# Kernel tuning notes

Measured on AMD Instinct MI355X. Metric: run time of the kernel, lower is better.

Reference implementation:

```python
import jax, jax.numpy as jnp
import numpy as np

B, P, D = 8, 4096, 3  # B point clouds, P points each, 3-D coords (code slices [:, :3])


def setup_inputs() -> dict:
    key = jax.random.key(0)
    k1, k2 = jax.random.split(key)
    y1 = jax.random.normal(k1, (B * P, D), dtype=jnp.float32)
    y2 = jax.random.normal(k2, (B * P, D), dtype=jnp.float32)
    # Sorted, equal-sized contiguous batch ids (as produced by PyG DataLoader batching).
    b1 = jnp.repeat(jnp.arange(B, dtype=jnp.int32), P)
    b2 = jnp.repeat(jnp.arange(B, dtype=jnp.int32), P)
    return {"y1": y1, "y2": y2, "b1": b1, "b2": b2}


def _chamfer(y1, y2):
    # Batch ids are contiguous with equal counts -> reshape to [B, P, D];
    # knn with batch args restricts neighbors to the same cloud.
    a = y1.reshape(B, P, D)
    c = y2.reshape(B, P, D)
    aa = jnp.sum(a * a, axis=-1)                      # [B, P]
    cc = jnp.sum(c * c, axis=-1)                      # [B, P]
    # Squared pairwise distances per cloud: [B, P, P]
    sq = aa[:, :, None] + cc[:, None, :] - 2.0 * jnp.einsum('bpd,bqd->bpq', a, c)
    # k=1 NN of each y1 point in y2 (argmin over y2 axis)
    idx1 = jnp.argmin(sq, axis=2)                     # [B, P]
    nn1 = jnp.take_along_axis(c, idx1[..., None], axis=1)  # [B, P, D]
    d1 = jnp.mean(jnp.linalg.norm(a - nn1, axis=-1))
    # k=1 NN of each y2 point in y1 (argmin over y1 axis)
    idx2 = jnp.argmin(sq, axis=1)                     # [B, P]
    nn2 = jnp.take_along_axis(a, idx2[..., None], axis=1)  # [B, P, D]
    d2 = jnp.mean(jnp.linalg.norm(c - nn2, axis=-1))
    return d1 + d2


def reference(y1, y2, b1, b2):
    # b1/b2 encode the contiguous equal-size batch structure assumed above.
    return _chamfer(y1, y2)
```

## Files before the change

kernel.cpp:

```cpp
#include <hip/hip_runtime.h>
#include <float.h>
#include <math.h>

#define BB 8
#define PP 4096

typedef __attribute__((ext_vector_type(8))) short bf16x8;
typedef __attribute__((ext_vector_type(16))) float f32x16;

__device__ __forceinline__ unsigned int f2bf(float f) {
    unsigned int u = __float_as_uint(f);
    return (u + 0x7FFFu + ((u >> 16) & 1u)) >> 16;
}
__device__ __forceinline__ float bf2f(unsigned int h) {
    return __uint_as_float(h << 16);
}
__device__ __forceinline__ float min3f(float a, float b, float c) {
    return fminf(fminf(a, b), c);
}

__global__ __launch_bounds__(1024) void chamfer_mfma(
    const float* __restrict__ y1, const float* __restrict__ y2,
    float* __restrict__ partial)
{
    __shared__ uint4 fbuf[64 * 64];

    const int bid   = blockIdx.x;
    const int qg    = bid & 15;
    const int cloud = (bid >> 4) & 7;
    const int dir   = bid >> 7;

    const float* src = (dir == 0) ? y1 : y2;
    const float* tgt = (dir == 0) ? y2 : y1;
    const float* __restrict__ tgt_base = tgt + (size_t)cloud * PP * 3;
    const float* __restrict__ src_base = src + ((size_t)cloud * PP + (size_t)qg * 256) * 3;

    const int tid  = threadIdx.x;
    const int lane = tid & 63;
    const int w    = tid >> 6;
    const int ig   = w & 1;
    const int jg   = w >> 1;

    bf16x8 bfrag[4];
    #pragma unroll
    for (int t = 0; t < 4; ++t) {
        const int ql = (ig * 4 + t) * 32 + (lane & 31);
        const float ax = src_base[ql * 3 + 0];
        const float ay = src_base[ql * 3 + 1];
        const float az = src_base[ql * 3 + 2];
        const unsigned int hx = f2bf(-ax), hy = f2bf(-ay), hz = f2bf(-az);
        const unsigned int lx = f2bf(-ax - bf2f(hx));
        const unsigned int ly = f2bf(-ay - bf2f(hy));
        const unsigned int lz = f2bf(-az - bf2f(hz));
        uint4 bb;
        if (lane < 32) {
            bb.x = hx | (hy << 16);
            bb.y = hz | (lx << 16);
            bb.z = ly | (lz << 16);
            bb.w = hx | (hy << 16);
        } else {
            bb.x = hz | (0x3F80u << 16);
            bb.y = 0x3F80u;
            bb.z = 0u;
            bb.w = 0u;
        }
        bfrag[t] = *reinterpret_cast<bf16x8*>(&bb);
    }

    float m[4][4];
    #pragma unroll
    for (int t = 0; t < 4; ++t)
        #pragma unroll
        for (int r = 0; r < 4; ++r)
            m[t][r] = FLT_MAX;

    f32x16 zc;
    #pragma unroll
    for (int r = 0; r < 16; ++r) zc[r] = 0.0f;

    for (int half = 0; half < 2; ++half) {
        #pragma unroll
        for (int rep = 0; rep < 2; ++rep) {
            const int nl = rep * 1024 + tid;
            const int n  = half * 2048 + nl;
            const float cx = tgt_base[n * 3 + 0];
            const float cy = tgt_base[n * 3 + 1];
            const float cz = tgt_base[n * 3 + 2];
            const unsigned int chx = f2bf(cx), chy = f2bf(cy), chz = f2bf(cz);
            const unsigned int clx = f2bf(cx - bf2f(chx));
            const unsigned int cly = f2bf(cy - bf2f(chy));
            const unsigned int clz = f2bf(cz - bf2f(chz));
            const float hh = 0.5f * (cx * cx + cy * cy + cz * cz);
            const unsigned int hhi = f2bf(hh);
            const unsigned int hlo = f2bf(hh - bf2f(hhi));
            const int tile = nl >> 5, r = nl & 31;
            uint4 lof, hif;
            lof.x = chx | (chy << 16);
            lof.y = chz | (chx << 16);
            lof.z = chy | (chz << 16);
            lof.w = clx | (cly << 16);
            hif.x = clz | (hhi << 16);
            hif.y = hlo;
            hif.z = 0u;
            hif.w = 0u;
            fbuf[tile * 64 + r]      = lof;
            fbuf[tile * 64 + 32 + r] = hif;
        }
        __syncthreads();

        for (int jt = jg * 8; jt < jg * 8 + 8; ++jt) {
            const bf16x8 af = *reinterpret_cast<const bf16x8*>(&fbuf[jt * 64 + lane]);
            #pragma unroll
            for (int t = 0; t < 4; ++t) {
                f32x16 acc = __builtin_amdgcn_mfma_f32_32x32x16_bf16(af, bfrag[t], zc, 0, 0, 0);
                m[t][0] = min3f(m[t][0], acc[0], acc[4]);
                m[t][1] = min3f(m[t][1], acc[1], acc[5]);
                m[t][2] = min3f(m[t][2], acc[2], acc[6]);
                m[t][3] = min3f(m[t][3], acc[3], acc[7]);
                m[t][0] = min3f(m[t][0], acc[8], acc[12]);
                m[t][1] = min3f(m[t][1], acc[9], acc[13]);
                m[t][2] = min3f(m[t][2], acc[10], acc[14]);
                m[t][3] = min3f(m[t][3], acc[11], acc[15]);
            }
        }
        __syncthreads();
    }

    float* pmin = reinterpret_cast<float*>(fbuf);
    float* ssum = pmin + 2048;
    #pragma unroll
    for (int t = 0; t < 4; ++t) {
        float mm = fminf(fminf(m[t][0], m[t][1]), fminf(m[t][2], m[t][3]));
        mm = fminf(mm, __shfl_xor(mm, 32));
        if (lane < 32)
            pmin[jg * 256 + (ig * 4 + t) * 32 + (lane & 31)] = mm;
    }
    __syncthreads();
    if (tid < 256) {
        float v = pmin[tid];
        #pragma unroll
        for (int g = 1; g < 8; ++g)
            v = fminf(v, pmin[g * 256 + tid]);
        const float ax = src_base[tid * 3 + 0];
        const float ay = src_base[tid * 3 + 1];
        const float az = src_base[tid * 3 + 2];
        const float aa = ax * ax + ay * ay + az * az;
        float d = sqrtf(fmaxf(0.0f, fmaf(2.0f, v, aa)));
        #pragma unroll
        for (int off = 32; off > 0; off >>= 1)
            d += __shfl_down(d, off);
        if ((tid & 63) == 0)
            ssum[tid >> 6] = d;
    }
    __syncthreads();
    if (tid == 0)
        partial[bid] = ssum[0] + ssum[1] + ssum[2] + ssum[3];
}

__global__ __launch_bounds__(256) void chamfer_final(
    const float* __restrict__ partial, float* __restrict__ out)
{
    __shared__ float ssum[4];
    const int tid = threadIdx.x;
    float v = partial[tid];
    #pragma unroll
    for (int off = 32; off > 0; off >>= 1)
        v += __shfl_down(v, off);
    if ((tid & 63) == 0)
        ssum[tid >> 6] = v;
    __syncthreads();
    if (tid == 0)
        out[0] = (ssum[0] + ssum[1] + ssum[2] + ssum[3]) * (1.0f / (float)(BB * PP));
}

extern "C" void kernel_launch(void* const* d_in, const int* in_sizes, int n_in,
                              void* d_out, int out_size, void* d_ws, size_t ws_size,
                              hipStream_t stream) {
    const float* y1 = (const float*)d_in[0];
    const float* y2 = (const float*)d_in[1];
    float* partial = (float*)d_ws;
    float* out     = (float*)d_out;

    chamfer_mfma<<<256, 1024, 0, stream>>>(y1, y2, partial);
    chamfer_final<<<1, 256, 0, stream>>>(partial, out);
}
```

Measured before the change: 17.96 us.

## Repartition warps so each owns one query tile and half the target tiles

```diff
diff --git a/kernel.cpp b/kernel.cpp
--- a/kernel.cpp
+++ b/kernel.cpp
@@ -38,13 +38,12 @@
     const int tid  = threadIdx.x;
     const int lane = tid & 63;
     const int w    = tid >> 6;
-    const int ig   = w & 1;
-    const int jg   = w >> 1;
+    const int ig   = w & 7;
+    const int jh   = w >> 3;
 
-    bf16x8 bfrag[4];
-    #pragma unroll
-    for (int t = 0; t < 4; ++t) {
-        const int ql = (ig * 4 + t) * 32 + (lane & 31);
+    bf16x8 bfrag;
+    {
+        const int ql = ig * 32 + (lane & 31);
         const float ax = src_base[ql * 3 + 0];
         const float ay = src_base[ql * 3 + 1];
         const float az = src_base[ql * 3 + 2];
@@ -64,15 +63,10 @@
             bb.z = 0u;
             bb.w = 0u;
         }
-        bfrag[t] = *reinterpret_cast<bf16x8*>(&bb);
+        bfrag = *reinterpret_cast<bf16x8*>(&bb);
     }
 
-    float m[4][4];
-    #pragma unroll
-    for (int t = 0; t < 4; ++t)
-        #pragma unroll
-        for (int r = 0; r < 4; ++r)
-            m[t][r] = FLT_MAX;
+    float m0 = FLT_MAX, m1 = FLT_MAX, m2 = FLT_MAX, m3 = FLT_MAX;
 
     f32x16 zc;
     #pragma unroll
@@ -108,39 +102,38 @@
         }
         __syncthreads();
 
-        for (int jt = jg * 8; jt < jg * 8 + 8; ++jt) {
-            const bf16x8 af = *reinterpret_cast<const bf16x8*>(&fbuf[jt * 64 + lane]);
-            #pragma unroll
-            for (int t = 0; t < 4; ++t) {
-                f32x16 acc = __builtin_amdgcn_mfma_f32_32x32x16_bf16(af, bfrag[t], zc, 0, 0, 0);
-                m[t][0] = min3f(m[t][0], acc[0], acc[4]);
-                m[t][1] = min3f(m[t][1], acc[1], acc[5]);
-                m[t][2] = min3f(m[t][2], acc[2], acc[6]);
-                m[t][3] = min3f(m[t][3], acc[3], acc[7]);
-                m[t][0] = min3f(m[t][0], acc[8], acc[12]);
-                m[t][1] = min3f(m[t][1], acc[9], acc[13]);
-                m[t][2] = min3f(m[t][2], acc[10], acc[14]);
-                m[t][3] = min3f(m[t][3], acc[11], acc[15]);
-            }
+        const int jt0 = jh * 32;
+        bf16x8 af = *reinterpret_cast<const bf16x8*>(&fbuf[jt0 * 64 + lane]);
+        #pragma unroll 4
+        for (int jt = 0; jt < 32; ++jt) {
+            bf16x8 afn = af;
+            if (jt < 31)
+                afn = *reinterpret_cast<const bf16x8*>(&fbuf[(jt0 + jt + 1) * 64 + lane]);
+            f32x16 acc = __builtin_amdgcn_mfma_f32_32x32x16_bf16(af, bfrag, zc, 0, 0, 0);
+            m0 = min3f(m0, acc[0], acc[4]);
+            m1 = min3f(m1, acc[1], acc[5]);
+            m2 = min3f(m2, acc[2], acc[6]);
+            m3 = min3f(m3, acc[3], acc[7]);
+            m0 = min3f(m0, acc[8], acc[12]);
+            m1 = min3f(m1, acc[9], acc[13]);
+            m2 = min3f(m2, acc[10], acc[14]);
+            m3 = min3f(m3, acc[11], acc[15]);
+            af = afn;
         }
         __syncthreads();
     }
 
     float* pmin = reinterpret_cast<float*>(fbuf);
-    float* ssum = pmin + 2048;
-    #pragma unroll
-    for (int t = 0; t < 4; ++t) {
-        float mm = fminf(fminf(m[t][0], m[t][1]), fminf(m[t][2], m[t][3]));
+    float* ssum = pmin + 512;
+    {
+        float mm = fminf(fminf(m0, m1), fminf(m2, m3));
         mm = fminf(mm, __shfl_xor(mm, 32));
         if (lane < 32)
-            pmin[jg * 256 + (ig * 4 + t) * 32 + (lane & 31)] = mm;
+            pmin[jh * 256 + ig * 32 + (lane & 31)] = mm;
     }
     __syncthreads();
     if (tid < 256) {
-        float v = pmin[tid];
-        #pragma unroll
-        for (int g = 1; g < 8; ++g)
-            v = fminf(v, pmin[g * 256 + tid]);
+        float v = fminf(pmin[tid], pmin[256 + tid]);
         const float ax = src_base[tid * 3 + 0];
         const float ay = src_base[tid * 3 + 1];
         const float az = src_base[tid * 3 + 2];
```

Result: no change. 17.97 us (+0.1%).

## Fuse final reduction via last-block atomic, halve block size, prefetch LDS fragments

Applied to the files above, without the earlier changes.

```diff
diff --git a/kernel.cpp b/kernel.cpp
--- a/kernel.cpp
+++ b/kernel.cpp
@@ -4,6 +4,9 @@
 
 #define BB 8
 #define PP 4096
+#define NBLK 512
+#define THREADS 512
+#define QB 128
 
 typedef __attribute__((ext_vector_type(8))) short bf16x8;
 typedef __attribute__((ext_vector_type(16))) float f32x16;
@@ -19,32 +22,31 @@
     return fminf(fminf(a, b), c);
 }
 
-__global__ __launch_bounds__(1024) void chamfer_mfma(
+__global__ __launch_bounds__(THREADS, 4) void chamfer_mfma(
     const float* __restrict__ y1, const float* __restrict__ y2,
-    float* __restrict__ partial)
+    float* __restrict__ partials, int* __restrict__ counter,
+    float* __restrict__ out)
 {
     __shared__ uint4 fbuf[64 * 64];
 
     const int bid   = blockIdx.x;
-    const int qg    = bid & 15;
-    const int cloud = (bid >> 4) & 7;
-    const int dir   = bid >> 7;
+    const int qg    = bid & 31;
+    const int cloud = (bid >> 5) & 7;
+    const int dir   = bid >> 8;
 
     const float* src = (dir == 0) ? y1 : y2;
     const float* tgt = (dir == 0) ? y2 : y1;
     const float* __restrict__ tgt_base = tgt + (size_t)cloud * PP * 3;
-    const float* __restrict__ src_base = src + ((size_t)cloud * PP + (size_t)qg * 256) * 3;
+    const float* __restrict__ src_base = src + ((size_t)cloud * PP + (size_t)qg * QB) * 3;
 
     const int tid  = threadIdx.x;
     const int lane = tid & 63;
-    const int w    = tid >> 6;
-    const int ig   = w & 1;
-    const int jg   = w >> 1;
+    const int jh   = tid >> 6;
 
     bf16x8 bfrag[4];
     #pragma unroll
     for (int t = 0; t < 4; ++t) {
-        const int ql = (ig * 4 + t) * 32 + (lane & 31);
+        const int ql = t * 32 + (lane & 31);
         const float ax = src_base[ql * 3 + 0];
         const float ay = src_base[ql * 3 + 1];
         const float az = src_base[ql * 3 + 2];
@@ -80,8 +82,8 @@
 
     for (int half = 0; half < 2; ++half) {
         #pragma unroll
-        for (int rep = 0; rep < 2; ++rep) {
-            const int nl = rep * 1024 + tid;
+        for (int rep = 0; rep < 4; ++rep) {
+            const int nl = rep * THREADS + tid;
             const int n  = half * 2048 + nl;
             const float cx = tgt_base[n * 3 + 0];
             const float cy = tgt_base[n * 3 + 1];
@@ -108,8 +110,12 @@
         }
         __syncthreads();
 
-        for (int jt = jg * 8; jt < jg * 8 + 8; ++jt) {
-            const bf16x8 af = *reinterpret_cast<const bf16x8*>(&fbuf[jt * 64 + lane]);
+        const int jt0 = jh * 8;
+        bf16x8 af = *reinterpret_cast<const bf16x8*>(&fbuf[jt0 * 64 + lane]);
+        for (int jt = 0; jt < 8; ++jt) {
+            bf16x8 afn = af;
+            if (jt < 7)
+                afn = *reinterpret_cast<const bf16x8*>(&fbuf[(jt0 + jt + 1) * 64 + lane]);
             #pragma unroll
             for (int t = 0; t < 4; ++t) {
                 f32x16 acc = __builtin_amdgcn_mfma_f32_32x32x16_bf16(af, bfrag[t], zc, 0, 0, 0);
@@ -122,25 +128,26 @@
                 m[t][2] = min3f(m[t][2], acc[10], acc[14]);
                 m[t][3] = min3f(m[t][3], acc[11], acc[15]);
             }
+            af = afn;
         }
         __syncthreads();
     }
 
     float* pmin = reinterpret_cast<float*>(fbuf);
-    float* ssum = pmin + 2048;
+    float* ssum = pmin + 8 * QB;
     #pragma unroll
     for (int t = 0; t < 4; ++t) {
         float mm = fminf(fminf(m[t][0], m[t][1]), fminf(m[t][2], m[t][3]));
         mm = fminf(mm, __shfl_xor(mm, 32));
         if (lane < 32)
-            pmin[jg * 256 + (ig * 4 + t) * 32 + (lane & 31)] = mm;
+            pmin[jh * QB + t * 32 + (lane & 31)] = mm;
     }
     __syncthreads();
-    if (tid < 256) {
+    if (tid < QB) {
         float v = pmin[tid];
         #pragma unroll
         for (int g = 1; g < 8; ++g)
-            v = fminf(v, pmin[g * 256 + tid]);
+            v = fminf(v, pmin[g * QB + tid]);
         const float ax = src_base[tid * 3 + 0];
         const float ay = src_base[tid * 3 + 1];
         const float az = src_base[tid * 3 + 2];
@@ -153,24 +160,28 @@
             ssum[tid >> 6] = d;
     }
     __syncthreads();
-    if (tid == 0)
-        partial[bid] = ssum[0] + ssum[1] + ssum[2] + ssum[3];
-}
 
-__global__ __launch_bounds__(256) void chamfer_final(
-    const float* __restrict__ partial, float* __restrict__ out)
-{
-    __shared__ float ssum[4];
-    const int tid = threadIdx.x;
-    float v = partial[tid];
-    #pragma unroll
-    for (int off = 32; off > 0; off >>= 1)
-        v += __shfl_down(v, off);
-    if ((tid & 63) == 0)
-        ssum[tid >> 6] = v;
+    __shared__ int lastflag;
+    if (tid == 0) {
+        partials[bid] = ssum[0] + ssum[1];
+        __threadfence();
+        const int ticket = atomicAdd(counter, 1);
+        lastflag = (ticket == NBLK - 1) ? 1 : 0;
+    }
     __syncthreads();
-    if (tid == 0)
-        out[0] = (ssum[0] + ssum[1] + ssum[2] + ssum[3]) * (1.0f / (float)(BB * PP));
+    if (lastflag && tid < 64) {
+        __threadfence();
+        float s = 0.0f;
+        #pragma unroll
+        for (int k = 0; k < NBLK / 64; ++k)
+            s += __hip_atomic_load(&partials[k * 64 + tid],
+                                   __ATOMIC_RELAXED, __HIP_MEMORY_SCOPE_AGENT);
+        #pragma unroll
+        for (int off = 32; off > 0; off >>= 1)
+            s += __shfl_down(s, off);
+        if (tid == 0)
+            out[0] = s * (1.0f / (float)(BB * PP));
+    }
 }
 
 extern "C" void kernel_launch(void* const* d_in, const int* in_sizes, int n_in,
@@ -178,9 +189,10 @@
                               hipStream_t stream) {
     const float* y1 = (const float*)d_in[0];
     const float* y2 = (const float*)d_in[1];
-    float* partial = (float*)d_ws;
-    float* out     = (float*)d_out;
+    float* partials = (float*)d_ws;
+    int*   counter  = (int*)((char*)d_ws + NBLK * 4);
+    float* out      = (float*)d_out;
 
-    chamfer_mfma<<<256, 1024, 0, stream>>>(y1, y2, partial);
-    chamfer_final<<<1, 256, 0, stream>>>(partial, out);
+    hipMemsetAsync(counter, 0, sizeof(int), stream);
+    chamfer_mfma<<<NBLK, THREADS, 0, stream>>>(y1, y2, partials, counter, out);
 }
```

Result: slower. 33.72 us (+87.7%).
